# Kernel optimization log

Measured on AMD Instinct MI355X. Metric: run time of the kernel, lower is better.

## Reference

```python
import jax, jax.numpy as jnp
import numpy as np

T, B, E = 1024, 4, 1024
H = 16
D = E // H          # head_dim = 64
L = 16              # max_relative_length


def setup_inputs() -> dict:
    key = jax.random.key(0)
    ks = jax.random.split(key, 4)
    query = jax.random.normal(ks[0], (T, B, E), dtype=jnp.float32)
    # xavier-ish scaled params
    in_proj_weight = jax.random.normal(ks[1], (3 * E, E), dtype=jnp.float32) * (1.0 / np.sqrt(E))
    in_proj_bias = jnp.zeros((3 * E,), dtype=jnp.float32)
    rel_pos_keys = jax.random.normal(ks[2], (2 * L + 1, E), dtype=jnp.float32) * (1.0 / np.sqrt(E))
    out_w = jax.random.normal(ks[3], (E, E), dtype=jnp.float32) * (1.0 / np.sqrt(E))
    out_b = jnp.zeros((E,), dtype=jnp.float32)
    return {"query": query, "in_proj_weight": in_proj_weight, "in_proj_bias": in_proj_bias,
            "rel_pos_keys": rel_pos_keys, "out_w": out_w, "out_b": out_b}


def reference(query, in_proj_weight, in_proj_bias, rel_pos_keys, out_w, out_b):
    t, b, e = query.shape
    scaling = D ** (-0.5)
    # fused qkv projection: [T,B,3E]
    qkv = jnp.einsum('tbe,fe->tbf', query, in_proj_weight) + in_proj_bias
    q, k, v = jnp.split(qkv, 3, axis=-1)
    q = q * scaling
    # [T,B,E] -> [B*H, T, D]
    def heads(x):
        return x.reshape(t, b * H, D).transpose(1, 0, 2)
    q, k, v = heads(q), heads(k), heads(v)
    # clipped relative position matrix [T,T] in [0, 2L]
    r = jnp.arange(t)
    dist = jnp.clip(r[None, :] - r[:, None], -L, L) + L
    # gather relation keys, keep first head_dim channels: [T,T,D]
    rel_k = rel_pos_keys[dist][:, :, :D]
    # scores = q k^T + q . rel_k  (Shaw et al.), [B*H, T, T]
    scores = jnp.einsum('btd,bsd->bts', q, k) + jnp.einsum('btd,tsd->bts', q, rel_k)
    probs = jax.nn.softmax(scores, axis=-1)
    attn = jnp.einsum('bts,bsd->btd', probs, v)      # [B*H, T, D]
    attn = attn.transpose(1, 0, 2).reshape(t, b, e)   # [T, B, E]
    return jnp.einsum('tbe,oe->tbo', attn, out_w) + out_b
```

## Files before the change

### kernel.cpp

```cpp
#include <hip/hip_runtime.h>

typedef __attribute__((ext_vector_type(8))) short short8;
typedef __attribute__((ext_vector_type(4))) float floatx4;


__device__ __forceinline__ short f2bf(float x) {
  union { float f; unsigned u; } cv; cv.f = x;
  unsigned u = cv.u + (0x7FFFu + ((cv.u >> 16) & 1u));
  return (short)(u >> 16);
}

__device__ __forceinline__ floatx4 mfma16(short8 a, short8 b, floatx4 c) {
  return __builtin_amdgcn_mfma_f32_16x16x32_bf16(a, b, c, 0, 0, 0);
}

__device__ __forceinline__ void async_copy16(const void* g, void* l) {
  __builtin_amdgcn_global_load_lds((const __attribute__((address_space(1))) void*)g,
                                   (__attribute__((address_space(3))) void*)l, 16, 0, 0);
}

__global__ void __launch_bounds__(256) f32_to_bf16_kernel(
    const float* __restrict__ src, short* __restrict__ dst, int n8)
{
  int i = blockIdx.x * 256 + threadIdx.x;
  if (i >= n8) return;
  const float4* s = (const float4*)src;
  float4 a = s[i * 2], b = s[i * 2 + 1];
  short8 o;
  o[0] = f2bf(a.x); o[1] = f2bf(a.y); o[2] = f2bf(a.z); o[3] = f2bf(a.w);
  o[4] = f2bf(b.x); o[5] = f2bf(b.y); o[6] = f2bf(b.z); o[7] = f2bf(b.w);
  *(short8*)(dst + (size_t)i * 8) = o;
}

__device__ __forceinline__ void gemm_stage(
    const short* __restrict__ A, const short* __restrict__ W,
    short* Atile, short* Btile, int m0, int n0, int K, int kk, int tid, int w)
{
  #pragma unroll
  for (int i = 0; i < 2; i++) {
    int seg = i * 256 + tid;
    int row = seg >> 2, c = seg & 3;
    async_copy16(A + (size_t)(m0 + row) * K + kk + c * 8,
                 Atile + (size_t)(i * 256 + w * 64) * 8);
    async_copy16(W + (size_t)(n0 + row) * K + kk + c * 8,
                 Btile + (size_t)(i * 256 + w * 64) * 8);
  }
}

__device__ __forceinline__ void gemm_core_db(
    const short* __restrict__ A, const short* __restrict__ W,
    short* At, short* Bt,
    int m0, int n0, int K, int tid, floatx4 acc[4][4])
{
  const int lane = tid & 63, w = tid >> 6;
  const int quad = lane >> 4, l16 = lane & 15;
  const int wm = (w >> 1) * 64, wn = (w & 1) * 64;
  #pragma unroll
  for (int mt = 0; mt < 4; mt++)
    #pragma unroll
    for (int nt = 0; nt < 4; nt++) acc[mt][nt] = (floatx4)(0.0f);

  gemm_stage(A, W, At, Bt, m0, n0, K, 0, tid, w);

  for (int kk = 0; kk < K; kk += 32) {
    const int cur = (kk >> 5) & 1;
    short* Ac = At + cur * (128 * 32);
    short* Bc = Bt + cur * (128 * 32);
    __syncthreads();
    if (kk + 32 < K)
      gemm_stage(A, W, At + (1 - cur) * (128 * 32), Bt + (1 - cur) * (128 * 32),
                 m0, n0, K, kk + 32, tid, w);
    short8 af[4], bfr[4];
    #pragma unroll
    for (int mt = 0; mt < 4; mt++)
      af[mt] = *(const short8*)(Ac + (wm + mt * 16 + l16) * 32 + quad * 8);
    #pragma unroll
    for (int nt = 0; nt < 4; nt++)
      bfr[nt] = *(const short8*)(Bc + (wn + nt * 16 + l16) * 32 + quad * 8);
    #pragma unroll
    for (int mt = 0; mt < 4; mt++)
      #pragma unroll
      for (int nt = 0; nt < 4; nt++)
        acc[mt][nt] = mfma16(af[mt], bfr[nt], acc[mt][nt]);
  }
}

__global__ void __launch_bounds__(256) gemm_qkv(
    const short* __restrict__ A, const short* __restrict__ W,
    const float* __restrict__ bias,
    short* __restrict__ q_ws, short* __restrict__ k_ws, short* __restrict__ v_ws)
{
  __shared__ __align__(16) short Atile[2 * 128 * 32];
  __shared__ __align__(16) short Btile[2 * 128 * 32];
  const int tid = threadIdx.x;
  const int m0 = blockIdx.x * 128, n0 = blockIdx.y * 128;
  floatx4 acc[4][4];
  gemm_core_db(A, W, Atile, Btile, m0, n0, 1024, tid, acc);

  const int lane = tid & 63, w = tid >> 6;
  const int quad = lane >> 4, l16 = lane & 15;
  const int wm = (w >> 1) * 64, wn = (w & 1) * 64;
  #pragma unroll
  for (int nt = 0; nt < 4; nt++) {
    int f = n0 + wn + nt * 16 + l16;
    float bv = bias[f];
    int which = f >> 10;
    int h = (f >> 6) & 15;
    int d = f & 63;
    #pragma unroll
    for (int mt = 0; mt < 4; mt++) {
      #pragma unroll
      for (int reg = 0; reg < 4; reg++) {
        int r = m0 + wm + mt * 16 + quad * 4 + reg;
        int t = r >> 2, b = r & 3;
        int bh = b * 16 + h;
        float val = acc[mt][nt][reg] + bv;
        if (which == 0)      q_ws[((size_t)bh * 1024 + t) * 64 + d] = f2bf(val * 0.125f);
        else if (which == 1) k_ws[((size_t)bh * 1024 + t) * 64 + d] = f2bf(val);
        else                 v_ws[((size_t)bh * 64 + d) * 1024 + t] = f2bf(val);
      }
    }
  }
}

__global__ void __launch_bounds__(256) attn_kernel(
    const short* __restrict__ q_ws, const short* __restrict__ k_ws,
    const short* __restrict__ v_ws, const float* __restrict__ relk,
    short* __restrict__ attn_ws)
{
  __shared__ float rel_lds[64 * 33];
  __shared__ __align__(16) short Ktile[2][64 * 64];
  __shared__ __align__(16) short Vtile[2][64 * 64];
  __shared__ __align__(16) short p_lds[4][16 * 64];
  const int tid = threadIdx.x, lane = tid & 63, w = tid >> 6;
  const int quad = lane >> 4, l16 = lane & 15;
  const int bh = blockIdx.x >> 4;
  const int t0 = (blockIdx.x & 15) * 64;
  const int b = bh >> 4, h = bh & 15;

  short8 aq[2];
  #pragma unroll
  for (int ks = 0; ks < 2; ks++)
    aq[ks] = *(const short8*)(q_ws + ((size_t)bh * 1024 + t0 + w * 16 + l16) * 64
                              + ks * 32 + quad * 8);

  for (int i = tid; i < 48 * 8; i += 256) {
    int row = i >> 3, p = i & 7;
    short8 val;
    if (row < 33) {
      const float* src = relk + row * 1024 + p * 8;
      float4 a = *(const float4*)src, c = *(const float4*)(src + 4);
      val[0] = f2bf(a.x); val[1] = f2bf(a.y); val[2] = f2bf(a.z); val[3] = f2bf(a.w);
      val[4] = f2bf(c.x); val[5] = f2bf(c.y); val[6] = f2bf(c.z); val[7] = f2bf(c.w);
    } else {
      val = (short8)0;
    }
    *(short8*)(Ktile[0] + row * 64 + ((p ^ (row & 7)) << 3)) = val;
  }
  __syncthreads();

  #pragma unroll
  for (int jt = 0; jt < 3; jt++) {
    floatx4 scR = (floatx4)(0.0f);
    #pragma unroll
    for (int ks = 0; ks < 2; ks++) {
      int rrow = jt * 16 + l16;
      int ck = (quad + 4 * ks) ^ (rrow & 7);
      short8 rb = *(const short8*)(Ktile[0] + rrow * 64 + ck * 8);
      scR = mfma16(aq[ks], rb, scR);
    }
    int j = jt * 16 + l16;
    if (j < 33) {
      #pragma unroll
      for (int reg = 0; reg < 4; reg++) {
        int tl = w * 16 + quad * 4 + reg;
        rel_lds[tl * 33 + j] = scR[reg];
      }
    }
  }
  __syncthreads();

  floatx4 o[4];
  #pragma unroll
  for (int dt = 0; dt < 4; dt++) o[dt] = (floatx4)(0.0f);
  float rsum[4] = {0.f, 0.f, 0.f, 0.f};

  float biasLo[4], biasHi[4];
  #pragma unroll
  for (int reg = 0; reg < 4; reg++) {
    int tl = w * 16 + quad * 4 + reg;
    biasLo[reg] = rel_lds[tl * 33 + 0];
    biasHi[reg] = rel_lds[tl * 33 + 32];
  }

  const short* kg = k_ws + (size_t)bh * 1024 * 64;
  const short* vg = v_ws + (size_t)bh * 64 * 1024;

  #define STAGE_KV(S0, BUF)                                                  \
    {                                                                        \
      _Pragma("unroll")                                                      \
      for (int i = 0; i < 2; i++) {                                          \
        int seg = i * 256 + tid;                                             \
        int row = seg >> 3, p = seg & 7;                                     \
        int ck = p ^ (row & 7);                                              \
        async_copy16(kg + (size_t)((S0) + row) * 64 + ck * 8,                \
                     Ktile[BUF] + (size_t)(i * 256 + w * 64) * 8);           \
        async_copy16(vg + (size_t)row * 1024 + (S0) + ck * 8,                \
                     Vtile[BUF] + (size_t)(i * 256 + w * 64) * 8);           \
      }                                                                      \
    }

  STAGE_KV(0, 0);

  for (int st = 0; st < 16; st++) {
    const int s0 = st * 64;
    const int cur = st & 1;
    __syncthreads();
    if (st < 15) STAGE_KV(s0 + 64, 1 - cur);

    floatx4 sc[4];
    #pragma unroll
    for (int nt = 0; nt < 4; nt++) {
      sc[nt] = (floatx4)(0.0f);
      #pragma unroll
      for (int ks = 0; ks < 2; ks++) {
        int srow = nt * 16 + l16;
        int ck = (quad + 4 * ks) ^ (l16 & 7);
        short8 kb = *(const short8*)(Ktile[cur] + srow * 64 + ck * 8);
        sc[nt] = mfma16(aq[ks], kb, sc[nt]);
      }
    }

    bool alllo = (s0 <= t0 + w * 16 - 79);
    bool allhi = (s0 >= t0 + w * 16 + 31);
    if (alllo || allhi) {
      #pragma unroll
      for (int reg = 0; reg < 4; reg++) {
        float bb = alllo ? biasLo[reg] : biasHi[reg];
        #pragma unroll
        for (int nt = 0; nt < 4; nt++) sc[nt][reg] += bb;
      }
    } else {
      #pragma unroll
      for (int nt = 0; nt < 4; nt++) {
        int s_glob = s0 + nt * 16 + l16;
        #pragma unroll
        for (int reg = 0; reg < 4; reg++) {
          int tl = w * 16 + quad * 4 + reg;
          int delta = min(max(s_glob - (t0 + tl), -16), 16) + 16;
          sc[nt][reg] += rel_lds[tl * 33 + delta];
        }
      }
    }

    #pragma unroll
    for (int nt = 0; nt < 4; nt++)
      #pragma unroll
      for (int reg = 0; reg < 4; reg++) {
        float p = __expf(sc[nt][reg]);
        sc[nt][reg] = p;
        rsum[reg] += p;
      }

    #pragma unroll
    for (int nt = 0; nt < 4; nt++)
      #pragma unroll
      for (int reg = 0; reg < 4; reg++) {
        int r = quad * 4 + reg;
        int cg = 2 * nt + (l16 >> 3);
        p_lds[w][r * 64 + ((cg ^ (r & 7)) << 3) + (l16 & 7)] = f2bf(sc[nt][reg]);
      }
    short8 ap[2];
    #pragma unroll
    for (int ks = 0; ks < 2; ks++) {
      int ck = (quad + 4 * ks) ^ (l16 & 7);
      ap[ks] = *(const short8*)(&p_lds[w][l16 * 64 + ck * 8]);
    }

    #pragma unroll
    for (int dt = 0; dt < 4; dt++) {
      #pragma unroll
      for (int ks = 0; ks < 2; ks++) {
        int drow = dt * 16 + l16;
        int ck = (quad + 4 * ks) ^ (l16 & 7);
        short8 vb = *(const short8*)(Vtile[cur] + drow * 64 + ck * 8);
        o[dt] = mfma16(ap[ks], vb, o[dt]);
      }
    }
  }
  #undef STAGE_KV

  #pragma unroll
  for (int reg = 0; reg < 4; reg++) {
    float rs = rsum[reg];
    #pragma unroll
    for (int off = 1; off < 16; off <<= 1) rs += __shfl_xor(rs, off, 64);
    rsum[reg] = 1.0f / rs;
  }
  #pragma unroll
  for (int dt = 0; dt < 4; dt++) {
    #pragma unroll
    for (int reg = 0; reg < 4; reg++) {
      int tg = t0 + w * 16 + quad * 4 + reg;
      attn_ws[((size_t)tg * 4 + b) * 1024 + h * 64 + dt * 16 + l16]
        = f2bf(o[dt][reg] * rsum[reg]);
    }
  }
}

__global__ void __launch_bounds__(256) gemm_outproj(
    const short* __restrict__ A, const short* __restrict__ W,
    const float* __restrict__ bias, float* __restrict__ out)
{
  __shared__ __align__(16) short Atile[2 * 128 * 32];
  __shared__ __align__(16) short Btile[2 * 128 * 32];
  const int tid = threadIdx.x;
  const int m0 = blockIdx.x * 128, n0 = blockIdx.y * 128;
  floatx4 acc[4][4];
  gemm_core_db(A, W, Atile, Btile, m0, n0, 1024, tid, acc);

  const int lane = tid & 63, w = tid >> 6;
  const int quad = lane >> 4, l16 = lane & 15;
  const int wm = (w >> 1) * 64, wn = (w & 1) * 64;
  #pragma unroll
  for (int nt = 0; nt < 4; nt++) {
    int f = n0 + wn + nt * 16 + l16;
    float bv = bias[f];
    #pragma unroll
    for (int mt = 0; mt < 4; mt++) {
      #pragma unroll
      for (int reg = 0; reg < 4; reg++) {
        int r = m0 + wm + mt * 16 + quad * 4 + reg;
        out[(size_t)r * 1024 + f] = acc[mt][nt][reg] + bv;
      }
    }
  }
}

extern "C" void kernel_launch(void* const* d_in, const int* in_sizes, int n_in,
                              void* d_out, int out_size, void* d_ws, size_t ws_size,
                              hipStream_t stream) {
  const float* query = (const float*)d_in[0];
  const float* in_w  = (const float*)d_in[1];
  const float* in_b  = (const float*)d_in[2];
  const float* relk  = (const float*)d_in[3];
  const float* out_w = (const float*)d_in[4];
  const float* out_b = (const float*)d_in[5];
  float* out = (float*)d_out;

  short* qry_bf = (short*)d_ws;
  short* win_bf = qry_bf + (size_t)4096 * 1024;
  short* wout_bf = win_bf + (size_t)3072 * 1024;
  short* q_ws   = wout_bf + (size_t)1024 * 1024;
  short* k_ws   = q_ws + (size_t)64 * 1024 * 64;
  short* v_ws   = k_ws + (size_t)64 * 1024 * 64;
  short* att_ws = v_ws + (size_t)64 * 1024 * 64;

  f32_to_bf16_kernel<<<4096 * 1024 / 8 / 256, 256, 0, stream>>>(query, qry_bf, 4096 * 1024 / 8);
  f32_to_bf16_kernel<<<3072 * 1024 / 8 / 256, 256, 0, stream>>>(in_w, win_bf, 3072 * 1024 / 8);
  f32_to_bf16_kernel<<<1024 * 1024 / 8 / 256, 256, 0, stream>>>(out_w, wout_bf, 1024 * 1024 / 8);

  gemm_qkv<<<dim3(32, 24), 256, 0, stream>>>(qry_bf, win_bf, in_b, q_ws, k_ws, v_ws);
  attn_kernel<<<1024, 256, 0, stream>>>(q_ws, k_ws, v_ws, relk, att_ws);
  gemm_outproj<<<dim3(32, 8), 256, 0, stream>>>(att_ws, wout_bf, out_b, out);
}
```

Measured before the change: 195.0 us.

## Fuse conversions, transpose attention score MFMA layout, shrink out-proj tiles

Merges the three fp32-to-bf16 conversion launches into one kernel that picks its source by index range, removing launch overhead. In attention, swaps the MFMA operands so each lane holds one query row. This simplifies the bias lookup and row-sum reduction and allows packed 8-byte P writes and reads with a rotation swizzle. The output projection now uses 64x128 tiles with its own double-buffered loop, doubling the grid to 512 blocks for better occupancy on the many CUs, at the cost of more B-tile reloads.

```diff
diff --git a/kernel.cpp b/kernel.cpp
--- a/kernel.cpp
+++ b/kernel.cpp
@@ -19,17 +19,22 @@
                                    (__attribute__((address_space(3))) void*)l, 16, 0, 0);
 }
 
-__global__ void __launch_bounds__(256) f32_to_bf16_kernel(
-    const float* __restrict__ src, short* __restrict__ dst, int n8)
+__global__ void __launch_bounds__(256) convert_all_kernel(
+    const float* __restrict__ s0, const float* __restrict__ s1,
+    const float* __restrict__ s2,
+    short* __restrict__ d0, short* __restrict__ d1, short* __restrict__ d2)
 {
   int i = blockIdx.x * 256 + threadIdx.x;
-  if (i >= n8) return;
+  const float* src; short* dst; int off;
+  if (i < 524288)       { src = s0; dst = d0; off = i; }
+  else if (i < 917504)  { src = s1; dst = d1; off = i - 524288; }
+  else                  { src = s2; dst = d2; off = i - 917504; }
   const float4* s = (const float4*)src;
-  float4 a = s[i * 2], b = s[i * 2 + 1];
+  float4 a = s[off * 2], b = s[off * 2 + 1];
   short8 o;
   o[0] = f2bf(a.x); o[1] = f2bf(a.y); o[2] = f2bf(a.z); o[3] = f2bf(a.w);
   o[4] = f2bf(b.x); o[5] = f2bf(b.y); o[6] = f2bf(b.z); o[7] = f2bf(b.w);
-  *(short8*)(dst + (size_t)i * 8) = o;
+  *(short8*)(dst + (size_t)off * 8) = o;
 }
 
 __device__ __forceinline__ void gemm_stage(
@@ -180,18 +185,14 @@
   }
   __syncthreads();
 
+  const int qloc = w * 16 + l16;
+  const float biasLo = rel_lds[qloc * 33 + 0];
+  const float biasHi = rel_lds[qloc * 33 + 32];
+
   floatx4 o[4];
   #pragma unroll
   for (int dt = 0; dt < 4; dt++) o[dt] = (floatx4)(0.0f);
-  float rsum[4] = {0.f, 0.f, 0.f, 0.f};
-
-  float biasLo[4], biasHi[4];
-  #pragma unroll
-  for (int reg = 0; reg < 4; reg++) {
-    int tl = w * 16 + quad * 4 + reg;
-    biasLo[reg] = rel_lds[tl * 33 + 0];
-    biasHi[reg] = rel_lds[tl * 33 + 32];
-  }
+  float rsum = 0.f;
 
   const short* kg = k_ws + (size_t)bh * 1024 * 64;
   const short* vg = v_ws + (size_t)bh * 64 * 1024;
@@ -227,54 +228,55 @@
         int srow = nt * 16 + l16;
         int ck = (quad + 4 * ks) ^ (l16 & 7);
         short8 kb = *(const short8*)(Ktile[cur] + srow * 64 + ck * 8);
-        sc[nt] = mfma16(aq[ks], kb, sc[nt]);
+        sc[nt] = mfma16(kb, aq[ks], sc[nt]);
       }
     }
 
     bool alllo = (s0 <= t0 + w * 16 - 79);
     bool allhi = (s0 >= t0 + w * 16 + 31);
     if (alllo || allhi) {
-      #pragma unroll
-      for (int reg = 0; reg < 4; reg++) {
-        float bb = alllo ? biasLo[reg] : biasHi[reg];
+      float bb = alllo ? biasLo : biasHi;
+      #pragma unroll
+      for (int nt = 0; nt < 4; nt++)
         #pragma unroll
-        for (int nt = 0; nt < 4; nt++) sc[nt][reg] += bb;
-      }
+        for (int reg = 0; reg < 4; reg++) sc[nt][reg] += bb;
     } else {
       #pragma unroll
       for (int nt = 0; nt < 4; nt++) {
-        int s_glob = s0 + nt * 16 + l16;
         #pragma unroll
         for (int reg = 0; reg < 4; reg++) {
-          int tl = w * 16 + quad * 4 + reg;
-          int delta = min(max(s_glob - (t0 + tl), -16), 16) + 16;
-          sc[nt][reg] += rel_lds[tl * 33 + delta];
+          int delta = (s0 + 16 * nt + 4 * quad + reg) - (t0 + qloc);
+          delta = min(max(delta, -16), 16) + 16;
+          sc[nt][reg] += rel_lds[qloc * 33 + delta];
         }
       }
     }
 
     #pragma unroll
-    for (int nt = 0; nt < 4; nt++)
+    for (int nt = 0; nt < 4; nt++) {
       #pragma unroll
       for (int reg = 0; reg < 4; reg++) {
         float p = __expf(sc[nt][reg]);
         sc[nt][reg] = p;
-        rsum[reg] += p;
-      }
-
-    #pragma unroll
-    for (int nt = 0; nt < 4; nt++)
-      #pragma unroll
-      for (int reg = 0; reg < 4; reg++) {
-        int r = quad * 4 + reg;
-        int cg = 2 * nt + (l16 >> 3);
-        p_lds[w][r * 64 + ((cg ^ (r & 7)) << 3) + (l16 & 7)] = f2bf(sc[nt][reg]);
-      }
+        rsum += p;
+      }
+      unsigned w0 = (unsigned)(unsigned short)f2bf(sc[nt][0])
+                  | ((unsigned)(unsigned short)f2bf(sc[nt][1]) << 16);
+      unsigned w1 = (unsigned)(unsigned short)f2bf(sc[nt][2])
+                  | ((unsigned)(unsigned short)f2bf(sc[nt][3]) << 16);
+      int srot = (16 * nt + 4 * quad + 4 * l16) & 63;
+      *(uint2*)(p_lds[w] + l16 * 64 + srot) = make_uint2(w0, w1);
+    }
+
     short8 ap[2];
     #pragma unroll
     for (int ks = 0; ks < 2; ks++) {
-      int ck = (quad + 4 * ks) ^ (l16 & 7);
-      ap[ks] = *(const short8*)(&p_lds[w][l16 * 64 + ck * 8]);
+      int s1 = (32 * ks + 8 * quad + 4 * l16) & 63;
+      int s2 = (s1 + 4) & 63;
+      union { short8 v; uint2 u[2]; } pu;
+      pu.u[0] = *(const uint2*)(p_lds[w] + l16 * 64 + s1);
+      pu.u[1] = *(const uint2*)(p_lds[w] + l16 * 64 + s2);
+      ap[ks] = pu.v;
     }
 
     #pragma unroll
@@ -290,20 +292,19 @@
   }
   #undef STAGE_KV
 
-  #pragma unroll
-  for (int reg = 0; reg < 4; reg++) {
-    float rs = rsum[reg];
-    #pragma unroll
-    for (int off = 1; off < 16; off <<= 1) rs += __shfl_xor(rs, off, 64);
-    rsum[reg] = 1.0f / rs;
-  }
+  rsum += __shfl_xor(rsum, 16, 64);
+  rsum += __shfl_xor(rsum, 32, 64);
+  float inv[4];
+  #pragma unroll
+  for (int reg = 0; reg < 4; reg++)
+    inv[reg] = 1.0f / __shfl(rsum, quad * 4 + reg, 64);
   #pragma unroll
   for (int dt = 0; dt < 4; dt++) {
     #pragma unroll
     for (int reg = 0; reg < 4; reg++) {
       int tg = t0 + w * 16 + quad * 4 + reg;
       attn_ws[((size_t)tg * 4 + b) * 1024 + h * 64 + dt * 16 + l16]
-        = f2bf(o[dt][reg] * rsum[reg]);
+        = f2bf(o[dt][reg] * inv[reg]);
     }
   }
 }
@@ -312,22 +313,64 @@
     const short* __restrict__ A, const short* __restrict__ W,
     const float* __restrict__ bias, float* __restrict__ out)
 {
-  __shared__ __align__(16) short Atile[2 * 128 * 32];
+  __shared__ __align__(16) short Atile[2 * 64 * 32];
   __shared__ __align__(16) short Btile[2 * 128 * 32];
   const int tid = threadIdx.x;
-  const int m0 = blockIdx.x * 128, n0 = blockIdx.y * 128;
-  floatx4 acc[4][4];
-  gemm_core_db(A, W, Atile, Btile, m0, n0, 1024, tid, acc);
-
+  const int m0 = blockIdx.x * 64, n0 = blockIdx.y * 128;
   const int lane = tid & 63, w = tid >> 6;
   const int quad = lane >> 4, l16 = lane & 15;
-  const int wm = (w >> 1) * 64, wn = (w & 1) * 64;
+  const int wm = (w >> 1) * 32, wn = (w & 1) * 64;
+
+  floatx4 acc[2][4];
+  #pragma unroll
+  for (int mt = 0; mt < 2; mt++)
+    #pragma unroll
+    for (int nt = 0; nt < 4; nt++) acc[mt][nt] = (floatx4)(0.0f);
+
+  #define STAGE_OP(KK, BUF)                                                  \
+    {                                                                        \
+      _Pragma("unroll")                                                      \
+      for (int i = 0; i < 2; i++) {                                          \
+        int seg = i * 256 + tid;                \
+        int row = seg >> 2, c = seg & 3;                                     \
+        async_copy16(W + (size_t)(n0 + row) * 1024 + (KK) + c * 8,           \
+                     Btile + (size_t)((BUF) * 4096 + (i * 256 + w * 64) * 8)); \
+      }                                                                      \
+      {                                                                      \
+        int row = tid >> 2, c = tid & 3;         \
+        async_copy16(A + (size_t)(m0 + row) * 1024 + (KK) + c * 8,           \
+                     Atile + (size_t)((BUF) * 2048 + (w * 64) * 8));         \
+      }                                                                      \
+    }
+
+  STAGE_OP(0, 0);
+  for (int kk = 0; kk < 1024; kk += 32) {
+    const int cur = (kk >> 5) & 1;
+    const short* Ac = Atile + cur * 2048;
+    const short* Bc = Btile + cur * 4096;
+    __syncthreads();
+    if (kk + 32 < 1024) STAGE_OP(kk + 32, 1 - cur);
+    short8 af[2], bfr[4];
+    #pragma unroll
+    for (int mt = 0; mt < 2; mt++)
+      af[mt] = *(const short8*)(Ac + (wm + mt * 16 + l16) * 32 + quad * 8);
+    #pragma unroll
+    for (int nt = 0; nt < 4; nt++)
+      bfr[nt] = *(const short8*)(Bc + (wn + nt * 16 + l16) * 32 + quad * 8);
+    #pragma unroll
+    for (int mt = 0; mt < 2; mt++)
+      #pragma unroll
+      for (int nt = 0; nt < 4; nt++)
+        acc[mt][nt] = mfma16(af[mt], bfr[nt], acc[mt][nt]);
+  }
+  #undef STAGE_OP
+
   #pragma unroll
   for (int nt = 0; nt < 4; nt++) {
     int f = n0 + wn + nt * 16 + l16;
     float bv = bias[f];
     #pragma unroll
-    for (int mt = 0; mt < 4; mt++) {
+    for (int mt = 0; mt < 2; mt++) {
       #pragma unroll
       for (int reg = 0; reg < 4; reg++) {
         int r = m0 + wm + mt * 16 + quad * 4 + reg;
@@ -356,11 +399,9 @@
   short* v_ws   = k_ws + (size_t)64 * 1024 * 64;
   short* att_ws = v_ws + (size_t)64 * 1024 * 64;
 
-  f32_to_bf16_kernel<<<4096 * 1024 / 8 / 256, 256, 0, stream>>>(query, qry_bf, 4096 * 1024 / 8);
-  f32_to_bf16_kernel<<<3072 * 1024 / 8 / 256, 256, 0, stream>>>(in_w, win_bf, 3072 * 1024 / 8);
-  f32_to_bf16_kernel<<<1024 * 1024 / 8 / 256, 256, 0, stream>>>(out_w, wout_bf, 1024 * 1024 / 8);
-
+  convert_all_kernel<<<4096, 256, 0, stream>>>(query, in_w, out_w,
+                                               qry_bf, win_bf, wout_bf);
   gemm_qkv<<<dim3(32, 24), 256, 0, stream>>>(qry_bf, win_bf, in_b, q_ws, k_ws, v_ws);
   attn_kernel<<<1024, 256, 0, stream>>>(q_ws, k_ws, v_ws, relk, att_ws);
-  gemm_outproj<<<dim3(32, 8), 256, 0, stream>>>(att_ws, wout_bf, out_b, out);
-}
+  gemm_outproj<<<dim3(64, 8), 256, 0, stream>>>(att_ws, wout_bf, out_b, out);
+}
```

Result: faster. 188.6 us (-3.3%).
